# Kernel tuning notes

Hardware: AMD Instinct MI355X
Metric: run time of the kernel (lower is better)

Reference implementation:

```python
import jax, jax.numpy as jnp
import numpy as np

CLASSES = 4
THETA = 0.5


def setup_inputs() -> dict:
    key = jax.random.key(0)
    k1, k2 = jax.random.split(key)
    f = jax.random.normal(k1, (2, 32, 48, 48), dtype=jnp.float32)
    p = jax.random.normal(k2, (2, 4, 48, 48), dtype=jnp.float32)
    return {"f": f, "p": p}


def reference(f, p):
    k_p = CLASSES / float(np.log(CLASSES))
    B, Cf, H, W = f.shape
    N = H * W
    # softmax over class dim, drop background channel -> [B, P, H, W], P = classes-1
    p = jax.nn.softmax(p, axis=1)[:, 1:, :, :]
    P = p.shape[1]
    f = f.reshape(B, Cf, N)   # [B, Cf, N]
    p = p.reshape(B, P, N)    # [B, P, N]

    # per-pixel channel statistics (torch .std is unbiased -> ddof=1)
    mu = f.mean(axis=1)           # [B, N]
    std = f.std(axis=1, ddof=1)   # [B, N]

    # symmetric Gaussian KL between every pixel pair (i = loop pixel, j = all)
    dmu2 = (mu[:, :, None] - mu[:, None, :]) ** 2          # [B, N, N]
    si2 = (std ** 2)[:, :, None]
    sj2 = (std ** 2)[:, None, :]
    log_ratio = jnp.log(std[:, None, :] / std[:, :, None]) + jnp.log(std[:, :, None] / std[:, None, :])
    KL = 0.5 * (log_ratio + (si2 + dmu2) / (2.0 * sj2) + (sj2 + dmu2) / (2.0 * si2) - 1.0)

    # cosine similarity between every pixel pair
    gram = jnp.einsum('bci,bcj->bij', f, f)                # [B, N, N]
    norm2 = (f ** 2).sum(axis=1)                           # [B, N]
    cos = gram / jnp.sqrt(norm2[:, :, None] * norm2[:, None, :])

    dist = (KL + 2.0 * (1.0 - cos)) / 3.0                  # [B, N, N]
    Wmat = jnp.exp(-dist ** 2 / THETA ** 2)                # affinity kernel

    # probability compatibility and entropy weights
    pi = p[:, :, :, None]  # loop pixel i
    pj = p[:, :, None, :]  # all pixels j
    A = jnp.abs(2.0 * pj * pi) / (pj ** 2 + pi ** 2)       # [B, P, N, N]
    E = 1.0 + k_p * p * jnp.log(p)                         # [B, P, N]
    G = A * E[:, :, :, None] * E[:, :, None, :]            # [B, P, N, N]

    # sum over loop pixel i, then mean over [B, P, N]
    total = jnp.einsum('bij,bkij->', Wmat, G)
    score = total / (B * P * N)
    return 1.0 - score / N
```

## Files before the change

### kernel.cpp

```cpp
#include <hip/hip_runtime.h>

#define NPIX 2304
#define BB   2
#define CF   32
#define NP   3
#define TILE 64
#define NT   (NPIX / TILE)
#define NTRI (NT * (NT + 1) / 2)
#define KP   2.885390081777927f

__device__ __forceinline__ float frcp(float x) { return __builtin_amdgcn_rcpf(x); }


__global__ void precompute_kernel(const float* __restrict__ f,
                                  const float* __restrict__ p,
                                  float* __restrict__ par,
                                  double* __restrict__ acc) {
    int idx = blockIdx.x * blockDim.x + threadIdx.x;
    if (idx == 0) *acc = 0.0;
    if (idx >= BB * NPIX) return;
    int b = idx / NPIX, n = idx % NPIX;

    const float* fb = f + (size_t)b * CF * NPIX + n;
    float s1 = 0.f, s2 = 0.f;
#pragma unroll
    for (int c = 0; c < CF; ++c) {
        float v = fb[(size_t)c * NPIX];
        s1 += v;
        s2 = fmaf(v, v, s2);
    }
    float mu  = s1 * (1.0f / CF);
    float var = (s2 - s1 * s1 * (1.0f / CF)) * (1.0f / (CF - 1));

    float* pb = par + ((size_t)b * 10) * NPIX + n;
    pb[0 * NPIX] = mu;
    pb[1 * NPIX] = var;
    pb[2 * NPIX] = 0.5f / var;
    pb[3 * NPIX] = rsqrtf(s2);

    const float* pp = p + (size_t)b * 4 * NPIX + n;
    float x0 = pp[0], x1 = pp[NPIX], x2 = pp[2 * NPIX], x3 = pp[3 * NPIX];
    float m  = fmaxf(fmaxf(x0, x1), fmaxf(x2, x3));
    float e0 = expf(x0 - m), e1 = expf(x1 - m), e2 = expf(x2 - m), e3 = expf(x3 - m);
    float inv = 1.0f / (e0 + e1 + e2 + e3);
    float q[3] = { e1 * inv, e2 * inv, e3 * inv };
#pragma unroll
    for (int k = 0; k < 3; ++k) {
        float qq = q[k];
        float E  = 1.0f + KP * qq * logf(qq);
        pb[(4 + k) * NPIX] = qq * E;
        pb[(7 + k) * NPIX] = qq * qq;
    }
}

__global__ __launch_bounds__(256) void pair_kernel(const float* __restrict__ f,
                                                   const float* __restrict__ par,
                                                   double* __restrict__ acc) {
    __shared__ float sFi[CF][TILE];
    __shared__ float sFj[CF][TILE];
    __shared__ float sPi[10][TILE];
    __shared__ float sPj[10][TILE];

    const int b = blockIdx.y;
    int rem = blockIdx.x, ti = 0;
    while (rem >= NT - ti) { rem -= NT - ti; ++ti; }
    const int tj = ti + rem;
    const int i0 = ti * TILE, j0 = tj * TILE;
    const int tid = threadIdx.x;

    {
        const float* fb = f + (size_t)b * CF * NPIX;
        int col = tid & 63, c0 = tid >> 6;
        for (int c = c0; c < CF; c += 4) {
            sFi[c][col] = fb[(size_t)c * NPIX + i0 + col];
            sFj[c][col] = fb[(size_t)c * NPIX + j0 + col];
        }
        const float* pb = par + (size_t)b * 10 * NPIX;
        for (int idx = tid; idx < 10 * TILE; idx += 256) {
            int r = idx >> 6, cc = idx & 63;
            sPi[r][cc] = pb[(size_t)r * NPIX + i0 + cc];
            sPj[r][cc] = pb[(size_t)r * NPIX + j0 + cc];
        }
    }
    __syncthreads();

    const int tx = tid & 15;
    const int ty = tid >> 4;

    float accv[4][4];
#pragma unroll
    for (int m = 0; m < 4; ++m)
#pragma unroll
        for (int n = 0; n < 4; ++n) accv[m][n] = 0.f;

#pragma unroll 8
    for (int c = 0; c < CF; ++c) {
        const float4 a4 = *(const float4*)&sFi[c][ty * 4];
        const float4 b4 = *(const float4*)&sFj[c][tx * 4];
        float ai[4] = { a4.x, a4.y, a4.z, a4.w };
        float bj[4] = { b4.x, b4.y, b4.z, b4.w };
#pragma unroll
        for (int m = 0; m < 4; ++m)
#pragma unroll
            for (int n = 0; n < 4; ++n)
                accv[m][n] = fmaf(ai[m], bj[n], accv[m][n]);
    }

    float pj[10][4];
#pragma unroll
    for (int r = 0; r < 10; ++r)
#pragma unroll
        for (int n = 0; n < 4; ++n) pj[r][n] = sPj[r][tx * 4 + n];

    float fsum = 0.f;
#pragma unroll
    for (int m = 0; m < 4; ++m) {
        const int ii = ty * 4 + m;
        const float mu_i = sPi[0][ii], si2_i = sPi[1][ii];
        const float h_i  = sPi[2][ii], rn_i  = sPi[3][ii];
        const float u_i0 = sPi[4][ii], u_i1 = sPi[5][ii], u_i2 = sPi[6][ii];
        const float s_i0 = sPi[7][ii], s_i1 = sPi[8][ii], s_i2 = sPi[9][ii];
#pragma unroll
        for (int n = 0; n < 4; ++n) {
            const float d    = mu_i - pj[0][n];
            const float dmu2 = d * d;
            const float KL   = 0.5f * ((si2_i + dmu2) * pj[2][n] + (pj[1][n] + dmu2) * h_i - 1.0f);
            const float cosv = accv[m][n] * rn_i * pj[3][n];
            const float dist = (KL + 2.0f - 2.0f * cosv) * (1.0f / 3.0f);
            const float wm   = __expf(-4.0f * dist * dist);
            const float g = 2.0f * ( u_i0 * pj[4][n] * frcp(s_i0 + pj[7][n])
                                   + u_i1 * pj[5][n] * frcp(s_i1 + pj[8][n])
                                   + u_i2 * pj[6][n] * frcp(s_i2 + pj[9][n]) );
            fsum = fmaf(wm, g, fsum);
        }
    }

    double sum = (double)fsum;
    for (int off = 32; off; off >>= 1) sum += __shfl_down(sum, off);
    __shared__ double wsumd[4];
    const int lane = tid & 63, wid = tid >> 6;
    if (lane == 0) wsumd[wid] = sum;
    __syncthreads();
    if (tid == 0) {
        const double wgt = (ti == tj) ? 1.0 : 2.0;
        double t = (wsumd[0] + wsumd[1]) + (wsumd[2] + wsumd[3]);
        atomicAdd(acc, t * wgt);
    }
}

__global__ void finalize_kernel(const double* __restrict__ acc, float* __restrict__ out) {
    out[0] = (float)(1.0 - acc[0] / ((double)BB * NP * (double)NPIX * (double)NPIX));
}

extern "C" void kernel_launch(void* const* d_in, const int* in_sizes, int n_in,
                              void* d_out, int out_size, void* d_ws, size_t ws_size,
                              hipStream_t stream) {
    const float* f = (const float*)d_in[0];
    const float* p = (const float*)d_in[1];
    float*  par = (float*)d_ws;
    double* acc = (double*)((char*)d_ws + (size_t)10 * BB * NPIX * sizeof(float));
    float*  out = (float*)d_out;

    precompute_kernel<<<(BB * NPIX + 255) / 256, 256, 0, stream>>>(f, p, par, acc);
    dim3 grid(NTRI, BB);
    pair_kernel<<<grid, 256, 0, stream>>>(f, par, acc);
    finalize_kernel<<<1, 1, 0, stream>>>(acc, out);
}
```

Baseline: 81.89 us.

## Fuse per-pixel precompute into pair kernel and replace atomics with partial sums

Removes the separate precompute kernel and recomputes per-pixel statistics (mean, variance, norms, softmax entropy terms) inside each pair tile from the shared-memory feature tile. The global atomicAdd into a zeroed accumulator is replaced by per-block partial sums reduced by a 256-thread finalize kernel. This cuts one launch and its inter-kernel dependency, at the cost of redundant per-tile recomputation, an extra barrier, and half the threads idling during the stats phase.

```diff
diff --git a/kernel.cpp b/kernel.cpp
--- a/kernel.cpp
+++ b/kernel.cpp
@@ -11,51 +11,9 @@
 
 __device__ __forceinline__ float frcp(float x) { return __builtin_amdgcn_rcpf(x); }
 
-
-__global__ void precompute_kernel(const float* __restrict__ f,
-                                  const float* __restrict__ p,
-                                  float* __restrict__ par,
-                                  double* __restrict__ acc) {
-    int idx = blockIdx.x * blockDim.x + threadIdx.x;
-    if (idx == 0) *acc = 0.0;
-    if (idx >= BB * NPIX) return;
-    int b = idx / NPIX, n = idx % NPIX;
-
-    const float* fb = f + (size_t)b * CF * NPIX + n;
-    float s1 = 0.f, s2 = 0.f;
-#pragma unroll
-    for (int c = 0; c < CF; ++c) {
-        float v = fb[(size_t)c * NPIX];
-        s1 += v;
-        s2 = fmaf(v, v, s2);
-    }
-    float mu  = s1 * (1.0f / CF);
-    float var = (s2 - s1 * s1 * (1.0f / CF)) * (1.0f / (CF - 1));
-
-    float* pb = par + ((size_t)b * 10) * NPIX + n;
-    pb[0 * NPIX] = mu;
-    pb[1 * NPIX] = var;
-    pb[2 * NPIX] = 0.5f / var;
-    pb[3 * NPIX] = rsqrtf(s2);
-
-    const float* pp = p + (size_t)b * 4 * NPIX + n;
-    float x0 = pp[0], x1 = pp[NPIX], x2 = pp[2 * NPIX], x3 = pp[3 * NPIX];
-    float m  = fmaxf(fmaxf(x0, x1), fmaxf(x2, x3));
-    float e0 = expf(x0 - m), e1 = expf(x1 - m), e2 = expf(x2 - m), e3 = expf(x3 - m);
-    float inv = 1.0f / (e0 + e1 + e2 + e3);
-    float q[3] = { e1 * inv, e2 * inv, e3 * inv };
-#pragma unroll
-    for (int k = 0; k < 3; ++k) {
-        float qq = q[k];
-        float E  = 1.0f + KP * qq * logf(qq);
-        pb[(4 + k) * NPIX] = qq * E;
-        pb[(7 + k) * NPIX] = qq * qq;
-    }
-}
-
 __global__ __launch_bounds__(256) void pair_kernel(const float* __restrict__ f,
-                                                   const float* __restrict__ par,
-                                                   double* __restrict__ acc) {
+                                                   const float* __restrict__ p,
+                                                   double* __restrict__ partial) {
     __shared__ float sFi[CF][TILE];
     __shared__ float sFj[CF][TILE];
     __shared__ float sPi[10][TILE];
@@ -75,11 +33,42 @@
             sFi[c][col] = fb[(size_t)c * NPIX + i0 + col];
             sFj[c][col] = fb[(size_t)c * NPIX + j0 + col];
         }
-        const float* pb = par + (size_t)b * 10 * NPIX;
-        for (int idx = tid; idx < 10 * TILE; idx += 256) {
-            int r = idx >> 6, cc = idx & 63;
-            sPi[r][cc] = pb[(size_t)r * NPIX + i0 + cc];
-            sPj[r][cc] = pb[(size_t)r * NPIX + j0 + cc];
+    }
+    __syncthreads();
+
+    if (tid < 128) {
+        const int side = tid >> 6;
+        const int col  = tid & 63;
+        const float (*sF)[TILE] = side ? sFj : sFi;
+        float (*sP)[TILE]       = side ? sPj : sPi;
+        const int base = (side ? j0 : i0) + col;
+
+        float s1 = 0.f, s2 = 0.f;
+#pragma unroll
+        for (int c = 0; c < CF; ++c) {
+            float v = sF[c][col];
+            s1 += v;
+            s2 = fmaf(v, v, s2);
+        }
+        float mu  = s1 * (1.0f / CF);
+        float var = (s2 - s1 * s1 * (1.0f / CF)) * (1.0f / (CF - 1));
+        sP[0][col] = mu;
+        sP[1][col] = var;
+        sP[2][col] = 0.5f / var;
+        sP[3][col] = rsqrtf(s2);
+
+        const float* pp = p + (size_t)b * 4 * NPIX + base;
+        float x0 = pp[0], x1 = pp[NPIX], x2 = pp[2 * NPIX], x3 = pp[3 * NPIX];
+        float m  = fmaxf(fmaxf(x0, x1), fmaxf(x2, x3));
+        float e0 = expf(x0 - m), e1 = expf(x1 - m), e2 = expf(x2 - m), e3 = expf(x3 - m);
+        float inv = 1.0f / (e0 + e1 + e2 + e3);
+        float q[3] = { e1 * inv, e2 * inv, e3 * inv };
+#pragma unroll
+        for (int k = 0; k < 3; ++k) {
+            float qq = q[k];
+            float E  = 1.0f + KP * qq * logf(qq);
+            sP[4 + k][col] = qq * E;
+            sP[7 + k][col] = qq * qq;
         }
     }
     __syncthreads();
@@ -143,13 +132,24 @@
     __syncthreads();
     if (tid == 0) {
         const double wgt = (ti == tj) ? 1.0 : 2.0;
-        double t = (wsumd[0] + wsumd[1]) + (wsumd[2] + wsumd[3]);
-        atomicAdd(acc, t * wgt);
+        partial[(size_t)b * NTRI + blockIdx.x] =
+            ((wsumd[0] + wsumd[1]) + (wsumd[2] + wsumd[3])) * wgt;
     }
 }
 
-__global__ void finalize_kernel(const double* __restrict__ acc, float* __restrict__ out) {
-    out[0] = (float)(1.0 - acc[0] / ((double)BB * NP * (double)NPIX * (double)NPIX));
+__global__ __launch_bounds__(256) void finalize_kernel(const double* __restrict__ partial,
+                                                       float* __restrict__ out) {
+    double s = 0.0;
+    for (int i = threadIdx.x; i < BB * NTRI; i += 256) s += partial[i];
+    for (int off = 32; off; off >>= 1) s += __shfl_down(s, off);
+    __shared__ double wsumd[4];
+    const int lane = threadIdx.x & 63, wid = threadIdx.x >> 6;
+    if (lane == 0) wsumd[wid] = s;
+    __syncthreads();
+    if (threadIdx.x == 0) {
+        double total = (wsumd[0] + wsumd[1]) + (wsumd[2] + wsumd[3]);
+        out[0] = (float)(1.0 - total / ((double)BB * NP * (double)NPIX * (double)NPIX));
+    }
 }
 
 extern "C" void kernel_launch(void* const* d_in, const int* in_sizes, int n_in,
@@ -157,12 +157,10 @@
                               hipStream_t stream) {
     const float* f = (const float*)d_in[0];
     const float* p = (const float*)d_in[1];
-    float*  par = (float*)d_ws;
-    double* acc = (double*)((char*)d_ws + (size_t)10 * BB * NPIX * sizeof(float));
-    float*  out = (float*)d_out;
+    double* partial = (double*)d_ws;
+    float*  out     = (float*)d_out;
 
-    precompute_kernel<<<(BB * NPIX + 255) / 256, 256, 0, stream>>>(f, p, par, acc);
     dim3 grid(NTRI, BB);
-    pair_kernel<<<grid, 256, 0, stream>>>(f, par, acc);
-    finalize_kernel<<<1, 1, 0, stream>>>(acc, out);
+    pair_kernel<<<grid, 256, 0, stream>>>(f, p, partial);
+    finalize_kernel<<<1, 256, 0, stream>>>(partial, out);
 }
```

Result: faster. 71.06 us (-13.2%).
